# Kernel optimization log

Measured on AMD Instinct MI355X. Metric: run time of the kernel, lower is better.

## Reference

```python
import jax, jax.numpy as jnp
import numpy as np

B, S, D, H = 4, 2048, 1024, 16
HD = D // H
EPS = 1e-7  # K.epsilon()


def setup_inputs() -> dict:
    key = jax.random.key(0)
    ks = jax.random.split(key, 5)
    scale = 1.0 / np.sqrt(D)  # keep projections numerically tame (glorot-ish)
    return {
        "x": jax.random.normal(ks[0], (B, S, D), dtype=jnp.float32),
        "Wq": jax.random.normal(ks[1], (D, D), dtype=jnp.float32) * scale,
        "bq": jnp.zeros((D,), dtype=jnp.float32),
        "Wk": jax.random.normal(ks[2], (D, D), dtype=jnp.float32) * scale,
        "bk": jnp.zeros((D,), dtype=jnp.float32),
        "Wv": jax.random.normal(ks[3], (D, D), dtype=jnp.float32) * scale,
        "bv": jnp.zeros((D,), dtype=jnp.float32),
        "Wo": jax.random.normal(ks[4], (D, D), dtype=jnp.float32) * scale,
        "bo": jnp.zeros((D,), dtype=jnp.float32),
    }


def _split_heads(t):
    # [B,S,D] -> [B,H,S,HD]
    return t.reshape(B, S, H, HD).transpose(0, 2, 1, 3)


def reference(x, Wq, bq, Wk, bk, Wv, bv, Wo, bo):
    relu = jax.nn.relu
    # projections with post-activation (keras layer applies activation to each mapping)
    q = _split_heads(relu(x @ Wq + bq))
    k = _split_heads(relu(x @ Wk + bk))
    v = _split_heads(relu(x @ Wv + bv))
    # scaled dot-product scores, scale = sqrt(head_dim)
    e = jnp.einsum("bhqd,bhkd->bhqk", q, k) / jnp.sqrt(jnp.asarray(HD, x.dtype))
    # exp with row max over ALL keys (before masking), as in the source
    e = jnp.exp(e - jnp.max(e, axis=-1, keepdims=True))
    # history_only: multiplicative causal mask applied AFTER exp
    causal = (jnp.arange(S)[None, :] <= jnp.arange(S)[:, None]).astype(x.dtype)
    e = e * causal  # broadcasts over [B,H,S,S]
    a = e / (jnp.sum(e, axis=-1, keepdims=True) + EPS)
    ctx = jnp.einsum("bhqk,bhkd->bhqd", a, v)
    y = ctx.transpose(0, 2, 1, 3).reshape(B, S, D)  # merge heads
    return relu(y @ Wo + bo)
```

## Files before the change

kernel.cpp:

```cpp
#include <hip/hip_runtime.h>
#include <hip/hip_bf16.h>
#include <cstdint>
#include <cstddef>

#define B_  4
#define S_  2048
#define D_  1024
#define H_  16
#define HD_ 64

typedef _Float16 half8  __attribute__((ext_vector_type(8)));
typedef _Float16 half4v __attribute__((ext_vector_type(4)));
typedef _Float16 half2v __attribute__((ext_vector_type(2)));
typedef float    f32x4  __attribute__((ext_vector_type(4)));
typedef unsigned int uint2v __attribute__((ext_vector_type(2)));
typedef unsigned int uint4v __attribute__((ext_vector_type(4)));

__device__ __forceinline__ void async_copy16(const void* g, void* l) {
    __builtin_amdgcn_global_load_lds(
        (const __attribute__((address_space(1))) unsigned int*)g,
        (__attribute__((address_space(3))) unsigned int*)l,
        16, 0, 0);
}

__device__ __forceinline__ half8 hscale8(half8 v, _Float16 s) {
    #pragma unroll
    for (int i = 0; i < 8; ++i) v[i] *= s;
    return v;
}

__device__ __forceinline__ unsigned int pack2(float a, float b) {
    half2v h = { (_Float16)a, (_Float16)b };
    return __builtin_bit_cast(unsigned int, h);
}


__global__ void cast_x_kernel(const float4* __restrict__ in, half4v* __restrict__ out, int n4) {
    int i = blockIdx.x * 256 + threadIdx.x;
    if (i < n4) {
        float4 v = in[i];
        half4v h = { (_Float16)v.x, (_Float16)v.y, (_Float16)v.z, (_Float16)v.w };
        out[i] = h;
    }
}

__global__ void transpose_cast4_kernel(
    const float* __restrict__ W0, const float* __restrict__ W1,
    const float* __restrict__ W2, const float* __restrict__ W3,
    _Float16* __restrict__ T0, _Float16* __restrict__ T1,
    _Float16* __restrict__ T2, _Float16* __restrict__ T3)
{
    __shared__ float tile[32][33];
    const float* Wsel[4] = { W0, W1, W2, W3 };
    _Float16*    Tsel[4] = { T0, T1, T2, T3 };
    const float* W  = Wsel[blockIdx.z];
    _Float16*    Wt = Tsel[blockIdx.z];
    const int bn = blockIdx.x * 32, bk = blockIdx.y * 32;
    const int tx = threadIdx.x, ty = threadIdx.y;
    #pragma unroll
    for (int i = 0; i < 32; i += 8)
        tile[ty + i][tx] = W[(size_t)(bk + ty + i) * D_ + bn + tx];
    __syncthreads();
    #pragma unroll
    for (int i = 0; i < 32; i += 8)
        Wt[(size_t)(bn + ty + i) * D_ + bk + tx] = (_Float16)tile[tx][ty + i];
}

template<int OUT_MODE>
__global__ __launch_bounds__(256, 2) void gemm_bt_kernel(
    const _Float16* __restrict__ A, const _Float16* __restrict__ Bt,
    const float* __restrict__ b0, const float* __restrict__ b1,
    const float* __restrict__ b2,
    void* __restrict__ C0, void* __restrict__ C1, void* __restrict__ C2,
    int M, int N, int K)
{
    __shared__ _Float16 As[128 * 64];
    __shared__ _Float16 Bs[128 * 64];
    const int tid  = threadIdx.x;
    const int wid  = tid >> 6, lane = tid & 63;
    const int lr   = lane & 15, lq = lane >> 4;
    const int m0   = blockIdx.x * 128, n0 = blockIdx.y * 128;
    const int wm   = (wid >> 1) * 64, wn = (wid & 1) * 64;
    const int srow = tid >> 3;
    const int csw  = ((tid & 7) ^ (srow & 7)) * 8;

    f32x4 acc[4][4] = {};

    for (int k0 = 0; k0 < K; k0 += 64) {
        __syncthreads();
        #pragma unroll
        for (int i = 0; i < 4; ++i) {
            async_copy16(A  + (size_t)(m0 + i * 32 + srow) * K + k0 + csw,
                         (char*)As + (i * 256 + wid * 64) * 16);
            async_copy16(Bt + (size_t)(n0 + i * 32 + srow) * K + k0 + csw,
                         (char*)Bs + (i * 256 + wid * 64) * 16);
        }
        __syncthreads();
        #pragma unroll
        for (int ks = 0; ks < 2; ++ks) {
            half8 af[4], bf[4];
            #pragma unroll
            for (int t = 0; t < 4; ++t) {
                af[t] = *(const half8*)(As + (wm + t * 16 + lr) * 64 + (((ks * 4 + lq) ^ (lr & 7)) * 8));
                bf[t] = *(const half8*)(Bs + (wn + t * 16 + lr) * 64 + (((ks * 4 + lq) ^ (lr & 7)) * 8));
            }
            #pragma unroll
            for (int mt = 0; mt < 4; ++mt)
                #pragma unroll
                for (int nt = 0; nt < 4; ++nt)
                    acc[mt][nt] = __builtin_amdgcn_mfma_f32_16x16x32_f16(
                        af[mt], bf[nt], acc[mt][nt], 0, 0, 0);
        }
    }

    const int seg = (OUT_MODE == 3) ? (n0 >> 10) : 0;
    const float* bp = (OUT_MODE == 3) ? (seg == 0 ? b0 : (seg == 1 ? b1 : b2)) : b0;

    #pragma unroll
    for (int mt = 0; mt < 4; ++mt) {
        const int row = m0 + wm + mt * 16 + lq * 4;
        #pragma unroll
        for (int nt = 0; nt < 4; ++nt) {
            const int col = n0 + wn + nt * 16 + lr;
            const int cl  = (OUT_MODE == 3) ? (col & 1023) : col;
            const float bb = bp[cl];
            if (OUT_MODE == 3 && seg == 2) {
                const int b = row >> 11, sq = row & 2047;
                const int h = cl >> 6, hd = cl & 63;
                half4v o;
                #pragma unroll
                for (int r = 0; r < 4; ++r) {
                    float v = acc[mt][nt][r] + bb;
                    o[r] = (_Float16)(v > 0.0f ? v : 0.0f);
                }
                *(half4v*)((_Float16*)C2 +
                           ((size_t)(b * 16 + h) * 64 + hd) * S_ + sq) = o;
            } else if (OUT_MODE == 3) {
                _Float16* dst = (_Float16*)(seg ? C1 : C0);
                #pragma unroll
                for (int r = 0; r < 4; ++r) {
                    float v = acc[mt][nt][r] + bb;
                    dst[(size_t)(row + r) * 1024 + cl] = (_Float16)(v > 0.0f ? v : 0.0f);
                }
            } else {
                #pragma unroll
                for (int r = 0; r < 4; ++r) {
                    float v = acc[mt][nt][r] + bb;
                    ((float*)C0)[(size_t)(row + r) * N + col] = v > 0.0f ? v : 0.0f;
                }
            }
        }
    }
}

__global__ __launch_bounds__(256, 2) void attn_kernel(
    const _Float16* __restrict__ Qg, const _Float16* __restrict__ Kg,
    const _Float16* __restrict__ Vtg, _Float16* __restrict__ Y)
{
    __shared__ _Float16 Ks[2][128 * 64];
    __shared__ _Float16 Vt[2][2][64 * 64];

    const int i  = blockIdx.x;
    const int bh = ((i & 7) << 3) | (i >> 6);
    const int praw = (i >> 3) & 7;
    const int p  = ((i >> 8) & 1) ? 7 - praw : praw;
    const int b  = bh >> 4, h = bh & 15;
    const int tid = threadIdx.x, wid = tid >> 6, lane = tid & 63;
    const int lr = lane & 15, lq = lane >> 4;

    const size_t base  = ((size_t)b * S_) * D_ + (size_t)h * HD_;
    const _Float16* Vh = Vtg + (size_t)bh * 64 * S_;

    const int srow = tid >> 3;
    const int csw  = ((tid & 7) ^ (srow & 7)) * 8;

    const int L = 128 * p, Hh = 1920 - 128 * p;
    const int qb[4] = { L + 16 * wid, L + 64 + 16 * wid,
                        Hh + 16 * wid, Hh + 64 + 16 * wid };
    const int dk[4] = { 2 * p, 2 * p + 1, 30 - 2 * p, 31 - 2 * p };
    const int nSuper = 16 - p;

    half8 aq[4][2];
    #pragma unroll
    for (int f = 0; f < 4; ++f) {
        const _Float16* qp = Qg + base + (size_t)(qb[f] + lr) * D_;
        aq[f][0] = hscale8(*(const half8*)(qp + lq * 8),      (_Float16)0.18033688f);
        aq[f][1] = hscale8(*(const half8*)(qp + 32 + lq * 8), (_Float16)0.18033688f);
    }

    float lsum[4] = {};
    f32x4 O[4][4] = {};

    auto issue_super = [&](int sb) {
        const int bufi = sb & 1;
        #pragma unroll
        for (int ii = 0; ii < 4; ++ii)
            async_copy16(Kg + base + (size_t)(sb * 128 + ii * 32 + srow) * D_ + csw,
                         (char*)Ks[bufi] + (ii * 256 + wid * 64) * 16);
        #pragma unroll
        for (int hh = 0; hh < 2; ++hh)
            #pragma unroll
            for (int ii = 0; ii < 2; ++ii)
                async_copy16(Vh + (size_t)(ii * 32 + srow) * S_ + sb * 128 + hh * 64 + csw,
                             (char*)Vt[bufi][hh] + (ii * 256 + wid * 64) * 16);
    };

    issue_super(0);

    for (int sb = 0; sb < nSuper; ++sb) {
        const int cur = sb & 1;
        __syncthreads();
        if (sb + 1 < nSuper) issue_super(sb + 1);

        const _Float16* Kc = Ks[cur];

        #pragma unroll
        for (int hh = 0; hh < 2; ++hh) {
            const int kb = sb * 2 + hh;
            const _Float16* Vc = Vt[cur][hh];

            half8 kf[2][4], bv[2][4];
            #pragma unroll
            for (int ks = 0; ks < 2; ++ks)
                #pragma unroll
                for (int tt = 0; tt < 4; ++tt) {
                    kf[ks][tt] = *(const half8*)(Kc + (hh * 64 + tt * 16 + lr) * 64
                                                 + (((ks * 4 + lq) ^ (lr & 7)) * 8));
                    bv[ks][tt] = *(const half8*)(Vc + (tt * 16 + lr) * 64
                                                 + (((ks * 4 + lq) ^ (lr & 7)) * 8));
                }

            #pragma unroll
            for (int f = 0; f < 4; ++f) {
                if (kb > dk[f]) continue;

                f32x4 sc[4];
                #pragma unroll
                for (int tt = 0; tt < 4; ++tt)
                    sc[tt] = f32x4{ -5.770780f, -5.770780f, -5.770780f, -5.770780f };
                __builtin_amdgcn_s_setprio(1);
                #pragma unroll
                for (int ks = 0; ks < 2; ++ks)
                    #pragma unroll
                    for (int tt = 0; tt < 4; ++tt)
                        sc[tt] = __builtin_amdgcn_mfma_f32_16x16x32_f16(kf[ks][tt], aq[f][ks], sc[tt], 0, 0, 0);
                __builtin_amdgcn_s_setprio(0);

                const bool diag = (kb == dk[f]);
                const int qg = qb[f] + lr;
                const int kbase = kb * 64 + lq * 4;
                float sum = 0.0f;
                unsigned int pk[4][2];
                #pragma unroll
                for (int tt = 0; tt < 4; ++tt) {
                    float ev[4];
                    #pragma unroll
                    for (int r = 0; r < 4; ++r) {
                        float e = __builtin_amdgcn_exp2f(fminf(sc[tt][r], 15.8696f));
                        if (diag)
                            e = (kbase + tt * 16 + r <= qg) ? e : 0.0f;
                        ev[r] = e;
                        sum += e;
                    }
                    pk[tt][0] = pack2(ev[0], ev[1]);
                    pk[tt][1] = pack2(ev[2], ev[3]);
                }
                lsum[f] += sum;

                half8 ap[2];
                #pragma unroll
                for (int ks = 0; ks < 2; ++ks) {
                    uint2v s1 = __builtin_amdgcn_permlane32_swap(pk[2 * ks][0], pk[2 * ks + 1][0], false, false);
                    uint2v s2 = __builtin_amdgcn_permlane16_swap(s1[0], s1[1], false, false);
                    uint2v u1 = __builtin_amdgcn_permlane32_swap(pk[2 * ks][1], pk[2 * ks + 1][1], false, false);
                    uint2v u2 = __builtin_amdgcn_permlane16_swap(u1[0], u1[1], false, false);
                    uint4v d = { s2[0], u2[0], s2[1], u2[1] };
                    ap[ks] = __builtin_bit_cast(half8, d);
                }

                __builtin_amdgcn_s_setprio(1);
                #pragma unroll
                for (int ks = 0; ks < 2; ++ks)
                    #pragma unroll
                    for (int tt = 0; tt < 4; ++tt)
                        O[f][tt] = __builtin_amdgcn_mfma_f32_16x16x32_f16(ap[ks], bv[ks][tt], O[f][tt], 0, 0, 0);
                __builtin_amdgcn_s_setprio(0);
            }
        }
    }

    #pragma unroll
    for (int f = 0; f < 4; ++f) {
        float tot = lsum[f];
        tot += __shfl_xor(tot, 16);
        tot += __shfl_xor(tot, 32);
        const int q0 = qb[f] + lq * 4;
        #pragma unroll
        for (int r = 0; r < 4; ++r) {
            const float inv = 1.0f / (__shfl(tot, lq * 4 + r) + 1e-7f);
            #pragma unroll
            for (int nt = 0; nt < 4; ++nt)
                Y[base + (size_t)(q0 + r) * D_ + nt * 16 + lr] = (_Float16)(O[f][nt][r] * inv);
        }
    }
}


extern "C" void kernel_launch(void* const* d_in, const int* in_sizes, int n_in,
                              void* d_out, int out_size, void* d_ws, size_t ws_size,
                              hipStream_t stream) {
    const float* x  = (const float*)d_in[0];
    const float* Wq = (const float*)d_in[1];
    const float* bq = (const float*)d_in[2];
    const float* Wk = (const float*)d_in[3];
    const float* bk = (const float*)d_in[4];
    const float* Wv = (const float*)d_in[5];
    const float* bv = (const float*)d_in[6];
    const float* Wo = (const float*)d_in[7];
    const float* bo = (const float*)d_in[8];

    char* ws = (char*)d_ws;
    _Float16* xh  = (_Float16*)ws;
    _Float16* wtq = (_Float16*)(ws + (size_t)16777216);
    _Float16* wtk = wtq + 1048576;
    _Float16* wtv = wtk + 1048576;
    _Float16* wto = wtv + 1048576;
    _Float16* Qh  = (_Float16*)(ws + (size_t)16777216 + 4 * (size_t)2097152);
    _Float16* Kh  = Qh + 8388608;
    _Float16* Vth = Kh + 8388608;
    _Float16* Yh  = Vth + 8388608;
    float* out = (float*)d_out;

    cast_x_kernel<<<8192, 256, 0, stream>>>((const float4*)x, (half4v*)xh, 2097152);
    transpose_cast4_kernel<<<dim3(32, 32, 4), dim3(32, 8), 0, stream>>>(
        Wq, Wk, Wv, Wo, wtq, wtk, wtv, wto);

    gemm_bt_kernel<3><<<dim3(64, 24), 256, 0, stream>>>(
        xh, wtq, bq, bk, bv, Qh, Kh, Vth, 8192, 3072, 1024);

    attn_kernel<<<512, 256, 0, stream>>>(Qh, Kh, Vth, Yh);

    gemm_bt_kernel<0><<<dim3(64, 8), 256, 0, stream>>>(
        Yh, wto, bo, bo, bo, out, out, out, 8192, 1024, 1024);
}
```

Measured before the change: 248.2 us.

## Use 256x256 double-buffered pipelined GEMM for fused QKV projection

Replaces the 128x128 single-buffered QKV projection GEMM with a 512-thread 256x256-tile kernel. It double-buffers LDS and interleaves async global-to-LDS prefetch of the next K-slice with MFMA compute across four sub-phases, using explicit vmcnt waits, barriers and setprio. The goal is to hide global load latency and raise data reuse per tile. The cost is more LDS (128KB per block), which limits occupancy, and a grid of only 384 blocks, which may underfill the 256 CUs unevenly.

```diff
diff --git a/kernel.cpp b/kernel.cpp
--- a/kernel.cpp
+++ b/kernel.cpp
@@ -66,13 +66,10 @@
         Wt[(size_t)(bn + ty + i) * D_ + bk + tx] = (_Float16)tile[tx][ty + i];
 }
 
-template<int OUT_MODE>
 __global__ __launch_bounds__(256, 2) void gemm_bt_kernel(
     const _Float16* __restrict__ A, const _Float16* __restrict__ Bt,
-    const float* __restrict__ b0, const float* __restrict__ b1,
-    const float* __restrict__ b2,
-    void* __restrict__ C0, void* __restrict__ C1, void* __restrict__ C2,
-    int M, int N, int K)
+    const float* __restrict__ b0,
+    float* __restrict__ C0, int M, int N, int K)
 {
     __shared__ _Float16 As[128 * 64];
     __shared__ _Float16 Bs[128 * 64];
@@ -113,18 +110,137 @@
         }
     }
 
-    const int seg = (OUT_MODE == 3) ? (n0 >> 10) : 0;
-    const float* bp = (OUT_MODE == 3) ? (seg == 0 ? b0 : (seg == 1 ? b1 : b2)) : b0;
-
     #pragma unroll
     for (int mt = 0; mt < 4; ++mt) {
         const int row = m0 + wm + mt * 16 + lq * 4;
         #pragma unroll
         for (int nt = 0; nt < 4; ++nt) {
             const int col = n0 + wn + nt * 16 + lr;
-            const int cl  = (OUT_MODE == 3) ? (col & 1023) : col;
+            const float bb = b0[col];
+            #pragma unroll
+            for (int r = 0; r < 4; ++r) {
+                float v = acc[mt][nt][r] + bb;
+                C0[(size_t)(row + r) * N + col] = v > 0.0f ? v : 0.0f;
+            }
+        }
+    }
+}
+
+__global__ __launch_bounds__(512, 2) void gemm256_qkv_kernel(
+    const _Float16* __restrict__ A, const _Float16* __restrict__ Bt,
+    const float* __restrict__ b0, const float* __restrict__ b1,
+    const float* __restrict__ b2,
+    _Float16* __restrict__ CQ, _Float16* __restrict__ CK,
+    _Float16* __restrict__ CV, int M, int N, int K)
+{
+    __shared__ _Float16 As[2][2][128 * 64];
+    __shared__ _Float16 Bs[2][2][128 * 64];
+
+    const int tid  = threadIdx.x;
+    const int wid  = tid >> 6, lane = tid & 63;
+    const int lr   = lane & 15, lq = lane >> 4;
+    const int m0   = blockIdx.x * 256, n0 = blockIdx.y * 256;
+    const int wm   = wid >> 2;
+    const int wn   = wid & 3;
+    const int bh   = wn >> 1;
+    const int brow0 = (wn & 1) * 64;
+
+    const int srow8 = lane >> 3;
+    const int csw8  = ((lane & 7) ^ srow8) * 8;
+
+    f32x4 acc[8][4] = {};
+
+    auto stageA = [&](int nxt, int k1, int h, int j) {
+        async_copy16(A + (size_t)(m0 + h * 128 + j * 64 + wid * 8 + srow8) * K + k1 + csw8,
+                     (char*)As[nxt][h] + j * 8192 + wid * 1024);
+    };
+    auto stageB = [&](int nxt, int k1, int h, int j) {
+        async_copy16(Bt + (size_t)(n0 + h * 128 + j * 64 + wid * 8 + srow8) * K + k1 + csw8,
+                     (char*)Bs[nxt][h] + j * 8192 + wid * 1024);
+    };
+
+    const int nk = K >> 6;
+
+    stageB(0, 0, 0, 0); stageB(0, 0, 0, 1);
+    stageB(0, 0, 1, 0); stageB(0, 0, 1, 1);
+    stageA(0, 0, 0, 0); stageA(0, 0, 1, 0);
+    stageA(0, 0, 0, 1); stageA(0, 0, 1, 1);
+    asm volatile("s_waitcnt vmcnt(0)" ::: "memory");
+    __builtin_amdgcn_s_barrier();
+
+    half8 bfr[4][2];
+
+    for (int t = 0; t < nk; ++t) {
+        const int buf = t & 1, nxt = buf ^ 1;
+        const int k1 = (t + 1) << 6;
+        const bool pf = (t + 1 < nk);
+        const _Float16* Ah = As[buf][wm];
+        const _Float16* Bh = Bs[buf][bh];
+
+        #pragma unroll
+        for (int q = 0; q < 4; ++q) {
+            if (q == 0) {
+                #pragma unroll
+                for (int nt = 0; nt < 4; ++nt)
+                    #pragma unroll
+                    for (int ks = 0; ks < 2; ++ks)
+                        bfr[nt][ks] = *(const half8*)(Bh + (brow0 + nt * 16 + lr) * 64
+                                                      + (((ks * 4 + lq) ^ (lr & 7)) * 8));
+            }
+            half8 afr[2][2];
+            #pragma unroll
+            for (int m2 = 0; m2 < 2; ++m2)
+                #pragma unroll
+                for (int ks = 0; ks < 2; ++ks)
+                    afr[m2][ks] = *(const half8*)(Ah + ((2 * q + m2) * 16 + lr) * 64
+                                                  + (((ks * 4 + lq) ^ (lr & 7)) * 8));
+
+            if (pf) {
+                if      (q == 0) { stageB(nxt, k1, 0, 0); stageB(nxt, k1, 0, 1); }
+                else if (q == 1) { stageB(nxt, k1, 1, 0); stageB(nxt, k1, 1, 1); }
+                else if (q == 2) { stageA(nxt, k1, 0, 0); stageA(nxt, k1, 1, 0); }
+                else             { stageA(nxt, k1, 0, 1); stageA(nxt, k1, 1, 1); }
+            }
+
+            asm volatile("" ::: "memory");
+            __builtin_amdgcn_s_barrier();
+            asm volatile("s_waitcnt lgkmcnt(0)" ::: "memory");
+
+            __builtin_amdgcn_s_setprio(1);
+            #pragma unroll
+            for (int m2 = 0; m2 < 2; ++m2)
+                #pragma unroll
+                for (int nt = 0; nt < 4; ++nt)
+                    #pragma unroll
+                    for (int ks = 0; ks < 2; ++ks)
+                        acc[2 * q + m2][nt] = __builtin_amdgcn_mfma_f32_16x16x32_f16(
+                            afr[m2][ks], bfr[nt][ks], acc[2 * q + m2][nt], 0, 0, 0);
+            __builtin_amdgcn_s_setprio(0);
+
+            if (q == 1) {
+                if (pf) asm volatile("s_waitcnt vmcnt(4)" ::: "memory");
+                else    asm volatile("s_waitcnt vmcnt(0)" ::: "memory");
+            }
+            if (q == 3)
+                asm volatile("s_waitcnt vmcnt(2)" ::: "memory");
+
+            asm volatile("" ::: "memory");
+            __builtin_amdgcn_s_barrier();
+        }
+    }
+
+    const int seg = n0 >> 10;
+    const float* bp = (seg == 0) ? b0 : (seg == 1 ? b1 : b2);
+
+    #pragma unroll
+    for (int mt = 0; mt < 8; ++mt) {
+        const int row = m0 + wm * 128 + mt * 16 + lq * 4;
+        #pragma unroll
+        for (int nt = 0; nt < 4; ++nt) {
+            const int col = n0 + wn * 64 + nt * 16 + lr;
+            const int cl  = col & 1023;
             const float bb = bp[cl];
-            if (OUT_MODE == 3 && seg == 2) {
+            if (seg == 2) {
                 const int b = row >> 11, sq = row & 2047;
                 const int h = cl >> 6, hd = cl & 63;
                 half4v o;
@@ -133,20 +249,13 @@
                     float v = acc[mt][nt][r] + bb;
                     o[r] = (_Float16)(v > 0.0f ? v : 0.0f);
                 }
-                *(half4v*)((_Float16*)C2 +
-                           ((size_t)(b * 16 + h) * 64 + hd) * S_ + sq) = o;
-            } else if (OUT_MODE == 3) {
-                _Float16* dst = (_Float16*)(seg ? C1 : C0);
+                *(half4v*)(CV + ((size_t)(b * 16 + h) * 64 + hd) * S_ + sq) = o;
+            } else {
+                _Float16* dst = seg ? CK : CQ;
                 #pragma unroll
                 for (int r = 0; r < 4; ++r) {
                     float v = acc[mt][nt][r] + bb;
                     dst[(size_t)(row + r) * 1024 + cl] = (_Float16)(v > 0.0f ? v : 0.0f);
-                }
-            } else {
-                #pragma unroll
-                for (int r = 0; r < 4; ++r) {
-                    float v = acc[mt][nt][r] + bb;
-                    ((float*)C0)[(size_t)(row + r) * N + col] = v > 0.0f ? v : 0.0f;
                 }
             }
         }
@@ -335,11 +444,11 @@
     transpose_cast4_kernel<<<dim3(32, 32, 4), dim3(32, 8), 0, stream>>>(
         Wq, Wk, Wv, Wo, wtq, wtk, wtv, wto);
 
-    gemm_bt_kernel<3><<<dim3(64, 24), 256, 0, stream>>>(
+    gemm256_qkv_kernel<<<dim3(32, 12), 512, 0, stream>>>(
         xh, wtq, bq, bk, bv, Qh, Kh, Vth, 8192, 3072, 1024);
 
     attn_kernel<<<512, 256, 0, stream>>>(Qh, Kh, Vth, Yh);
 
-    gemm_bt_kernel<0><<<dim3(64, 8), 256, 0, stream>>>(
-        Yh, wto, bo, bo, bo, out, out, out, 8192, 1024, 1024);
-}
+    gemm_bt_kernel<<<dim3(64, 8), 256, 0, stream>>>(
+        Yh, wto, bo, out, 8192, 1024, 1024);
+}
```

Measured after the change: 259.6 us. +4.6%, slower.
